# Optimization experiments

Hardware: AMD Instinct MI355X
Metric: run time of the kernel (lower is better)

## Reference

```python
import jax, jax.numpy as jnp
import numpy as np

NEG_SLOPE = 0.2  # LeakyReLU negative slope (act_negative)


def setup_inputs() -> dict:
    key = jax.random.key(0)
    ks = jax.random.split(key, 5)
    B, N, D = 64, 4096, 16
    x = jax.random.normal(ks[0], (B, N, D), dtype=jnp.float32)
    # random adjacency, scaled so row sums are O(1) and activations stay stable
    adj = jax.random.uniform(ks[1], (N, N), dtype=jnp.float32) * (2.0 / N)
    Identity = jnp.eye(N, dtype=jnp.float32)
    W0 = jax.random.normal(ks[2], (D, D), dtype=jnp.float32) * (1.0 / np.sqrt(D))
    W1 = jax.random.normal(ks[3], (D, D), dtype=jnp.float32) * (1.0 / np.sqrt(D))
    W2 = jax.random.normal(ks[4], (D, D), dtype=jnp.float32) * (1.0 / np.sqrt(D))
    return {"x": x, "adj": adj, "Identity": Identity, "W0": W0, "W1": W1, "W2": W2}


def _gcn_layer(x, W, adj, I):
    # GCNConv: linear (no bias) -> leaky_relu -> batched adjacency matmul.
    # The same conv (same W) is applied with adj and with Identity, then summed.
    h = jax.nn.leaky_relu(jnp.einsum('bnd,de->bne', x, W), NEG_SLOPE)
    out_adj = jnp.einsum('nm,bmh->bnh', adj, h)  # replaces per-sample torch.mm loop
    out_id = jnp.einsum('nm,bmh->bnh', I, h)
    return out_adj + out_id


def reference(x, adj, Identity, W0, W1, W2):
    out = _gcn_layer(x, W0, adj, Identity)
    out = _gcn_layer(out, W1, adj, Identity)
    out = _gcn_layer(out, W2, adj, Identity)
    return out  # is_residual=False: no shortcut branch
```

## Files before the change

kernel.cpp:

```cpp
#include <hip/hip_runtime.h>
#include <stdint.h>


typedef float  f32x4  __attribute__((ext_vector_type(4)));
typedef unsigned short ushort8 __attribute__((ext_vector_type(8)));
typedef long   i64x2  __attribute__((ext_vector_type(2)));

typedef __attribute__((address_space(1))) void* as1p;
typedef __attribute__((address_space(3))) void* as3p;
#define GLOAD_LDS16(G, L) \
  __builtin_amdgcn_global_load_lds((as1p)(G), (as3p)(L), 16, 0, 0)

#define P_ELEMS 4194304
#define ADJ_SCALE 4096.0f
#define ADJ_DESCALE (1.0f / 4096.0f)

__device__ __forceinline__ unsigned short f2bf(float f) {
  unsigned u = __float_as_uint(f);
  u += 0x7fffu + ((u >> 16) & 1u);
  return (unsigned short)(u >> 16);
}
__device__ __forceinline__ float bf2f(unsigned short u) {
  return __uint_as_float(((unsigned)u) << 16);
}
__device__ __forceinline__ int pk4_fp8(float a, float b, float c, float d) {
  int v = __builtin_amdgcn_cvt_pk_fp8_f32(a, b, 0, false);
  v = __builtin_amdgcn_cvt_pk_fp8_f32(c, d, v, true);
  return v;
}

__global__ void make_adj8(const float* __restrict__ adj,
                          unsigned char* __restrict__ a8) {
  size_t base = ((size_t)blockIdx.x * 256 + threadIdx.x) * 16;
  const float4* src = (const float4*)(adj + base);
  float4 q0 = src[0], q1 = src[1], q2 = src[2], q3 = src[3];
  int4 o;
  o.x = pk4_fp8(q0.x * ADJ_SCALE, q0.y * ADJ_SCALE, q0.z * ADJ_SCALE, q0.w * ADJ_SCALE);
  o.y = pk4_fp8(q1.x * ADJ_SCALE, q1.y * ADJ_SCALE, q1.z * ADJ_SCALE, q1.w * ADJ_SCALE);
  o.z = pk4_fp8(q2.x * ADJ_SCALE, q2.y * ADJ_SCALE, q2.z * ADJ_SCALE, q2.w * ADJ_SCALE);
  o.w = pk4_fp8(q3.x * ADJ_SCALE, q3.y * ADJ_SCALE, q3.z * ADJ_SCALE, q3.w * ADJ_SCALE);
  *(int4*)(a8 + base) = o;
}

__global__ void linear_fuse(const float* __restrict__ x,
                            const unsigned short* __restrict__ pp,
                            const unsigned short* __restrict__ hnc_in,
                            const float* __restrict__ W,
                            unsigned char* __restrict__ hb8,
                            unsigned short* __restrict__ hnc_out,
                            int mode) {
  __shared__ float xs[64 * 65];
  __shared__ unsigned short ht[64 * 72];
  int n0 = blockIdx.x * 64, c0 = blockIdx.y * 64;

  if (mode == 0) {
    for (int i = threadIdx.x; i < 1024; i += 256) {
      int bs = i >> 8, rem = i & 255, nr = rem >> 2, d4 = rem & 3;
      float4 v = *(const float4*)(
          x + ((size_t)(c0 / 16 + bs) * 4096 + n0 + nr) * 16 + d4 * 4);
      float* dst = xs + nr * 65 + bs * 16 + d4 * 4;
      dst[0] = v.x; dst[1] = v.y; dst[2] = v.z; dst[3] = v.w;
    }
  } else {
    for (int i = threadIdx.x; i < 512; i += 256) {
      int row = i >> 3, ch = i & 7;
      size_t g = (size_t)(n0 + row) * 1024 + c0 + ch * 8;
      ushort8 a = *(const ushort8*)(pp + g);
      ushort8 b = *(const ushort8*)(pp + P_ELEMS + g);
      ushort8 c = *(const ushort8*)(hnc_in + g);
      float* dst = xs + row * 65 + ch * 8;
#pragma unroll
      for (int j = 0; j < 8; ++j) dst[j] = bf2f(a[j]) + bf2f(b[j]) + bf2f(c[j]);
    }
  }
  __syncthreads();

  int n_l = threadIdx.x & 63, b_l = threadIdx.x >> 6;
  float xv[16];
#pragma unroll
  for (int d = 0; d < 16; ++d) xv[d] = xs[n_l * 65 + b_l * 16 + d];
  float accv[16];
#pragma unroll
  for (int e = 0; e < 16; ++e) accv[e] = 0.f;
#pragma unroll
  for (int d = 0; d < 16; ++d)
#pragma unroll
    for (int e = 0; e < 16; ++e) accv[e] += xv[d] * W[d * 16 + e];

  ushort8 h0, h1;
#pragma unroll
  for (int e = 0; e < 16; ++e) {
    float a = accv[e] > 0.f ? accv[e] : 0.2f * accv[e];
    unsigned short hv = f2bf(a);
    ht[(b_l * 16 + e) * 72 + n_l] = hv;
    if (e < 8) h0[e] = hv; else h1[e - 8] = hv;
  }
  unsigned short* ho = hnc_out + (size_t)(n0 + n_l) * 1024 + c0 + b_l * 16;
  *(ushort8*)(ho)     = h0;
  *(ushort8*)(ho + 8) = h1;
  __syncthreads();

  for (int i = threadIdx.x; i < 512; i += 256) {
    int row = i >> 3, ch = i & 7;
    const unsigned short* s = ht + row * 72 + ch * 8;
    int2 v;
    v.x = pk4_fp8(bf2f(s[0]), bf2f(s[1]), bf2f(s[2]), bf2f(s[3]));
    v.y = pk4_fp8(bf2f(s[4]), bf2f(s[5]), bf2f(s[6]), bf2f(s[7]));
    *(int2*)(hb8 + (size_t)(c0 + row) * 4096 + n0 + ch * 8) = v;
  }
}

__global__ void add_out(const unsigned short* __restrict__ pp,
                        const unsigned short* __restrict__ hnc,
                        float* __restrict__ out) {
  int gid = blockIdx.x * 256 + threadIdx.x;
  int n = gid >> 7, c8 = (gid & 127) * 8;
  size_t g = (size_t)n * 1024 + c8;
  ushort8 a = *(const ushort8*)(pp + g);
  ushort8 b = *(const ushort8*)(pp + P_ELEMS + g);
  ushort8 h = *(const ushort8*)(hnc + g);
  float v[8];
#pragma unroll
  for (int j = 0; j < 8; ++j) v[j] = bf2f(a[j]) + bf2f(b[j]) + bf2f(h[j]);
  int bb = c8 >> 4, d0 = c8 & 15;
  float* o = out + (size_t)bb * 65536 + n * 16 + d0;
  *(float4*)(o)     = float4{v[0], v[1], v[2], v[3]};
  *(float4*)(o + 4) = float4{v[4], v[5], v[6], v[7]};
}

__global__ __launch_bounds__(256, 2)
void gemm_f8(const unsigned char* __restrict__ A,
             const unsigned char* __restrict__ B8,
             unsigned short* __restrict__ pp) {
  const int K = 4096;
  __shared__ unsigned char a_s[128 * 128];
  __shared__ unsigned char b_s[128 * 128];

  int tid = threadIdx.x, wave = tid >> 6, lane = tid & 63;

  int lin = blockIdx.x;
  int xcd = lin & 7, g = lin >> 3;
  int mth = g & 3, ct = (g >> 2) & 7, ks = g >> 5;
  int mt = mth * 8 + xcd;
  int n0 = mt * 128, c0 = ct * 128;
  int kbase = ks * 2048;

  int l8 = lane >> 3, lc = lane & 7;
  int swc = lc ^ l8;
  const unsigned char* gA[4];
  const unsigned char* gB[4];
#pragma unroll
  for (int j = 0; j < 4; ++j) {
    int r = wave * 32 + j * 8 + l8;
    gA[j] = A  + (size_t)(n0 + r) * K + kbase + swc * 16;
    gB[j] = B8 + (size_t)(c0 + r) * K + kbase + swc * 16;
  }

  int i16 = lane & 15, q = lane >> 4;
  int wm = wave >> 1, wn = wave & 1;
  int sw7 = i16 & 7;

  f32x4 acc[4][4] = {};

  for (int it = 0; it < 16; ++it) {
    int k0 = it * 128;
    __syncthreads();
#pragma unroll
    for (int j = 0; j < 4; ++j) {
      GLOAD_LDS16(gA[j] + k0, a_s + (wave * 32 + j * 8) * 128);
      GLOAD_LDS16(gB[j] + k0, b_s + (wave * 32 + j * 8) * 128);
    }
    __syncthreads();
#pragma unroll
    for (int s = 0; s < 2; ++s) {
      int pc = ((s * 4 + q) ^ sw7) * 16;
      i64x2 bv[4];
#pragma unroll
      for (int u = 0; u < 4; ++u)
        bv[u] = *(const i64x2*)(b_s + (wn * 64 + u * 16 + i16) * 128 + pc);
#pragma unroll
      for (int t = 0; t < 4; ++t) {
        i64x2 av = *(const i64x2*)(a_s + (wm * 64 + t * 16 + i16) * 128 + pc);
#pragma unroll
        for (int u = 0; u < 4; ++u) {
          acc[t][u] = __builtin_amdgcn_mfma_f32_16x16x32_fp8_fp8(av.x, bv[u].x, acc[t][u], 0, 0, 0);
          acc[t][u] = __builtin_amdgcn_mfma_f32_16x16x32_fp8_fp8(av.y, bv[u].y, acc[t][u], 0, 0, 0);
        }
      }
    }
  }

  unsigned short* dst = pp + (size_t)ks * P_ELEMS;
#pragma unroll
  for (int t = 0; t < 4; ++t)
#pragma unroll
    for (int u = 0; u < 4; ++u)
#pragma unroll
      for (int i = 0; i < 4; ++i) {
        int n_g = n0 + wm * 64 + t * 16 + q * 4 + i;
        int c_g = c0 + wn * 64 + u * 16 + i16;
        dst[(size_t)n_g * 1024 + c_g] = f2bf(acc[t][u][i] * ADJ_DESCALE);
      }
}

extern "C" void kernel_launch(void* const* d_in, const int* in_sizes, int n_in,
                              void* d_out, int out_size, void* d_ws, size_t ws_size,
                              hipStream_t stream) {
  const float* x   = (const float*)d_in[0];
  const float* adj = (const float*)d_in[1];
  const float* W0  = (const float*)d_in[3];
  const float* W1  = (const float*)d_in[4];
  const float* W2  = (const float*)d_in[5];
  float* out = (float*)d_out;

  char* ws = (char*)d_ws;
  unsigned char*  adj8 = (unsigned char*)ws;
  unsigned char*  hb8  = (unsigned char*)(ws + 16777216);
  unsigned short* hnc  = (unsigned short*)(ws + 20971520);
  unsigned short* pp   = (unsigned short*)(ws + 29360128);

  make_adj8<<<4096, 256, 0, stream>>>(adj, adj8);

  linear_fuse<<<dim3(64, 16), 256, 0, stream>>>(x, pp, hnc, W0, hb8, hnc, 0);
  gemm_f8<<<512, 256, 0, stream>>>(adj8, hb8, pp);
  linear_fuse<<<dim3(64, 16), 256, 0, stream>>>(x, pp, hnc, W1, hb8, hnc, 1);
  gemm_f8<<<512, 256, 0, stream>>>(adj8, hb8, pp);
  linear_fuse<<<dim3(64, 16), 256, 0, stream>>>(x, pp, hnc, W2, hb8, hnc, 1);
  gemm_f8<<<512, 256, 0, stream>>>(adj8, hb8, pp);
  add_out<<<2048, 256, 0, stream>>>(pp, hnc, out);
}
```

Measured before the change: 262.5 us.

## Use scaled 16x16x128 FP8 MFMA and merge adjacency quantization with first linear

The GEMM inner loop now does each 128-wide K slice with one gfx950 scaled MFMA (16x16x128 f8f6f4, unit scales) instead of eight 16x16x32 FP8 MFMAs. Each lane loads two swizzled 16-byte chunks per row tile to build the 32-byte operand. Separately, the adjacency FP8 conversion and the first-layer linear are merged into one launch, with block index choosing the role, which removes one kernel launch. The risk is that the lane-to-K mapping of the new operand layout must match the instruction, and the merged kernel may use more shared memory per block than the conversion blocks need.

```diff
diff --git a/kernel.cpp b/kernel.cpp
--- a/kernel.cpp
+++ b/kernel.cpp
@@ -4,7 +4,8 @@
 
 typedef float  f32x4  __attribute__((ext_vector_type(4)));
 typedef unsigned short ushort8 __attribute__((ext_vector_type(8)));
-typedef long   i64x2  __attribute__((ext_vector_type(2)));
+typedef int    i32x4  __attribute__((ext_vector_type(4)));
+typedef int    i32x8  __attribute__((ext_vector_type(8)));
 
 typedef __attribute__((address_space(1))) void* as1p;
 typedef __attribute__((address_space(3))) void* as3p;
@@ -14,6 +15,7 @@
 #define P_ELEMS 4194304
 #define ADJ_SCALE 4096.0f
 #define ADJ_DESCALE (1.0f / 4096.0f)
+#define SCALE_ONE 0x7f7f7f7f
 
 __device__ __forceinline__ unsigned short f2bf(float f) {
   unsigned u = __float_as_uint(f);
@@ -29,49 +31,93 @@
   return v;
 }
 
-__global__ void make_adj8(const float* __restrict__ adj,
-                          unsigned char* __restrict__ a8) {
-  size_t base = ((size_t)blockIdx.x * 256 + threadIdx.x) * 16;
-  const float4* src = (const float4*)(adj + base);
-  float4 q0 = src[0], q1 = src[1], q2 = src[2], q3 = src[3];
-  int4 o;
-  o.x = pk4_fp8(q0.x * ADJ_SCALE, q0.y * ADJ_SCALE, q0.z * ADJ_SCALE, q0.w * ADJ_SCALE);
-  o.y = pk4_fp8(q1.x * ADJ_SCALE, q1.y * ADJ_SCALE, q1.z * ADJ_SCALE, q1.w * ADJ_SCALE);
-  o.z = pk4_fp8(q2.x * ADJ_SCALE, q2.y * ADJ_SCALE, q2.z * ADJ_SCALE, q2.w * ADJ_SCALE);
-  o.w = pk4_fp8(q3.x * ADJ_SCALE, q3.y * ADJ_SCALE, q3.z * ADJ_SCALE, q3.w * ADJ_SCALE);
-  *(int4*)(a8 + base) = o;
-}
-
-__global__ void linear_fuse(const float* __restrict__ x,
-                            const unsigned short* __restrict__ pp,
+__global__ void prep(const float* __restrict__ adj,
+                     unsigned char* __restrict__ a8,
+                     const float* __restrict__ x,
+                     const float* __restrict__ W,
+                     unsigned char* __restrict__ hb8,
+                     unsigned short* __restrict__ hnc_out) {
+  __shared__ float xs[64 * 65];
+  __shared__ unsigned short ht[64 * 72];
+  int bid = blockIdx.x;
+
+  if (bid >= 1024) {
+    size_t base = ((size_t)(bid - 1024) * 256 + threadIdx.x) * 16;
+    const float4* src = (const float4*)(adj + base);
+    float4 q0 = src[0], q1 = src[1], q2 = src[2], q3 = src[3];
+    int4 o;
+    o.x = pk4_fp8(q0.x * ADJ_SCALE, q0.y * ADJ_SCALE, q0.z * ADJ_SCALE, q0.w * ADJ_SCALE);
+    o.y = pk4_fp8(q1.x * ADJ_SCALE, q1.y * ADJ_SCALE, q1.z * ADJ_SCALE, q1.w * ADJ_SCALE);
+    o.z = pk4_fp8(q2.x * ADJ_SCALE, q2.y * ADJ_SCALE, q2.z * ADJ_SCALE, q2.w * ADJ_SCALE);
+    o.w = pk4_fp8(q3.x * ADJ_SCALE, q3.y * ADJ_SCALE, q3.z * ADJ_SCALE, q3.w * ADJ_SCALE);
+    *(int4*)(a8 + base) = o;
+    return;
+  }
+
+  int n0 = (bid & 63) * 64, c0 = (bid >> 6) * 64;
+
+  for (int i = threadIdx.x; i < 1024; i += 256) {
+    int bs = i >> 8, rem = i & 255, nr = rem >> 2, d4 = rem & 3;
+    float4 v = *(const float4*)(
+        x + ((size_t)(c0 / 16 + bs) * 4096 + n0 + nr) * 16 + d4 * 4);
+    float* dst = xs + nr * 65 + bs * 16 + d4 * 4;
+    dst[0] = v.x; dst[1] = v.y; dst[2] = v.z; dst[3] = v.w;
+  }
+  __syncthreads();
+
+  int n_l = threadIdx.x & 63, b_l = threadIdx.x >> 6;
+  float xv[16];
+#pragma unroll
+  for (int d = 0; d < 16; ++d) xv[d] = xs[n_l * 65 + b_l * 16 + d];
+  float accv[16];
+#pragma unroll
+  for (int e = 0; e < 16; ++e) accv[e] = 0.f;
+#pragma unroll
+  for (int d = 0; d < 16; ++d)
+#pragma unroll
+    for (int e = 0; e < 16; ++e) accv[e] += xv[d] * W[d * 16 + e];
+
+  ushort8 h0, h1;
+#pragma unroll
+  for (int e = 0; e < 16; ++e) {
+    float a = accv[e] > 0.f ? accv[e] : 0.2f * accv[e];
+    unsigned short hv = f2bf(a);
+    ht[(b_l * 16 + e) * 72 + n_l] = hv;
+    if (e < 8) h0[e] = hv; else h1[e - 8] = hv;
+  }
+  unsigned short* ho = hnc_out + (size_t)(n0 + n_l) * 1024 + c0 + b_l * 16;
+  *(ushort8*)(ho)     = h0;
+  *(ushort8*)(ho + 8) = h1;
+  __syncthreads();
+
+  for (int i = threadIdx.x; i < 512; i += 256) {
+    int row = i >> 3, ch = i & 7;
+    const unsigned short* s = ht + row * 72 + ch * 8;
+    int2 v;
+    v.x = pk4_fp8(bf2f(s[0]), bf2f(s[1]), bf2f(s[2]), bf2f(s[3]));
+    v.y = pk4_fp8(bf2f(s[4]), bf2f(s[5]), bf2f(s[6]), bf2f(s[7]));
+    *(int2*)(hb8 + (size_t)(c0 + row) * 4096 + n0 + ch * 8) = v;
+  }
+}
+
+__global__ void linear_fuse(const unsigned short* __restrict__ pp,
                             const unsigned short* __restrict__ hnc_in,
                             const float* __restrict__ W,
                             unsigned char* __restrict__ hb8,
-                            unsigned short* __restrict__ hnc_out,
-                            int mode) {
+                            unsigned short* __restrict__ hnc_out) {
   __shared__ float xs[64 * 65];
   __shared__ unsigned short ht[64 * 72];
   int n0 = blockIdx.x * 64, c0 = blockIdx.y * 64;
 
-  if (mode == 0) {
-    for (int i = threadIdx.x; i < 1024; i += 256) {
-      int bs = i >> 8, rem = i & 255, nr = rem >> 2, d4 = rem & 3;
-      float4 v = *(const float4*)(
-          x + ((size_t)(c0 / 16 + bs) * 4096 + n0 + nr) * 16 + d4 * 4);
-      float* dst = xs + nr * 65 + bs * 16 + d4 * 4;
-      dst[0] = v.x; dst[1] = v.y; dst[2] = v.z; dst[3] = v.w;
-    }
-  } else {
-    for (int i = threadIdx.x; i < 512; i += 256) {
-      int row = i >> 3, ch = i & 7;
-      size_t g = (size_t)(n0 + row) * 1024 + c0 + ch * 8;
-      ushort8 a = *(const ushort8*)(pp + g);
-      ushort8 b = *(const ushort8*)(pp + P_ELEMS + g);
-      ushort8 c = *(const ushort8*)(hnc_in + g);
-      float* dst = xs + row * 65 + ch * 8;
-#pragma unroll
-      for (int j = 0; j < 8; ++j) dst[j] = bf2f(a[j]) + bf2f(b[j]) + bf2f(c[j]);
-    }
+  for (int i = threadIdx.x; i < 512; i += 256) {
+    int row = i >> 3, ch = i & 7;
+    size_t g = (size_t)(n0 + row) * 1024 + c0 + ch * 8;
+    ushort8 a = *(const ushort8*)(pp + g);
+    ushort8 b = *(const ushort8*)(pp + P_ELEMS + g);
+    ushort8 c = *(const ushort8*)(hnc_in + g);
+    float* dst = xs + row * 65 + ch * 8;
+#pragma unroll
+    for (int j = 0; j < 8; ++j) dst[j] = bf2f(a[j]) + bf2f(b[j]) + bf2f(c[j]);
   }
   __syncthreads();
 
@@ -159,6 +205,8 @@
   int i16 = lane & 15, q = lane >> 4;
   int wm = wave >> 1, wn = wave & 1;
   int sw7 = i16 & 7;
+  int pc0 = ((2 * q) ^ sw7) * 16;
+  int pc1 = ((2 * q + 1) ^ sw7) * 16;
 
   f32x4 acc[4][4] = {};
 
@@ -171,22 +219,25 @@
       GLOAD_LDS16(gB[j] + k0, b_s + (wave * 32 + j * 8) * 128);
     }
     __syncthreads();
-#pragma unroll
-    for (int s = 0; s < 2; ++s) {
-      int pc = ((s * 4 + q) ^ sw7) * 16;
-      i64x2 bv[4];
+
+    i32x8 bv[4];
+#pragma unroll
+    for (int u = 0; u < 4; ++u) {
+      const unsigned char* bp = b_s + (wn * 64 + u * 16 + i16) * 128;
+      i32x4 blo = *(const i32x4*)(bp + pc0);
+      i32x4 bhi = *(const i32x4*)(bp + pc1);
+      bv[u] = __builtin_shufflevector(blo, bhi, 0, 1, 2, 3, 4, 5, 6, 7);
+    }
+#pragma unroll
+    for (int t = 0; t < 4; ++t) {
+      const unsigned char* ap = a_s + (wm * 64 + t * 16 + i16) * 128;
+      i32x4 alo = *(const i32x4*)(ap + pc0);
+      i32x4 ahi = *(const i32x4*)(ap + pc1);
+      i32x8 av = __builtin_shufflevector(alo, ahi, 0, 1, 2, 3, 4, 5, 6, 7);
 #pragma unroll
       for (int u = 0; u < 4; ++u)
-        bv[u] = *(const i64x2*)(b_s + (wn * 64 + u * 16 + i16) * 128 + pc);
-#pragma unroll
-      for (int t = 0; t < 4; ++t) {
-        i64x2 av = *(const i64x2*)(a_s + (wm * 64 + t * 16 + i16) * 128 + pc);
-#pragma unroll
-        for (int u = 0; u < 4; ++u) {
-          acc[t][u] = __builtin_amdgcn_mfma_f32_16x16x32_fp8_fp8(av.x, bv[u].x, acc[t][u], 0, 0, 0);
-          acc[t][u] = __builtin_amdgcn_mfma_f32_16x16x32_fp8_fp8(av.y, bv[u].y, acc[t][u], 0, 0, 0);
-        }
-      }
+        acc[t][u] = __builtin_amdgcn_mfma_scale_f32_16x16x128_f8f6f4(
+            av, bv[u], acc[t][u], 0, 0, 0, SCALE_ONE, 0, SCALE_ONE);
     }
   }
 
@@ -219,13 +270,11 @@
   unsigned short* hnc  = (unsigned short*)(ws + 20971520);
   unsigned short* pp   = (unsigned short*)(ws + 29360128);
 
-  make_adj8<<<4096, 256, 0, stream>>>(adj, adj8);
-
-  linear_fuse<<<dim3(64, 16), 256, 0, stream>>>(x, pp, hnc, W0, hb8, hnc, 0);
+  prep<<<5120, 256, 0, stream>>>(adj, adj8, x, W0, hb8, hnc);
   gemm_f8<<<512, 256, 0, stream>>>(adj8, hb8, pp);
-  linear_fuse<<<dim3(64, 16), 256, 0, stream>>>(x, pp, hnc, W1, hb8, hnc, 1);
+  linear_fuse<<<dim3(64, 16), 256, 0, stream>>>(pp, hnc, W1, hb8, hnc);
   gemm_f8<<<512, 256, 0, stream>>>(adj8, hb8, pp);
-  linear_fuse<<<dim3(64, 16), 256, 0, stream>>>(x, pp, hnc, W2, hb8, hnc, 1);
+  linear_fuse<<<dim3(64, 16), 256, 0, stream>>>(pp, hnc, W2, hb8, hnc);
   gemm_f8<<<512, 256, 0, stream>>>(adj8, hb8, pp);
   add_out<<<2048, 256, 0, stream>>>(pp, hnc, out);
 }
```

After: 244.7 us. 1.07x faster.
